# Kernel optimization log

Measured on AMD Instinct MI355X. Metric: run time of the kernel, lower is better.

Reference implementation:

```python
import jax, jax.numpy as jnp
import numpy as np

N_SRC, N_DST, K = 50000, 10000, 32
IN_F, OUT_F, H, L = 256, 128, 8, 10


def setup_inputs() -> dict:
    key = jax.random.key(0)
    ks = jax.random.split(key, 12)
    s = 0.05
    return {
        "feat": jax.random.normal(ks[0], (N_SRC, IN_F), jnp.float32),
        "labels": jax.random.uniform(ks[1], (N_SRC, L), jnp.float32),
        "labels_ori": jax.random.uniform(ks[2], (N_SRC, L), jnp.float32),
        "label_rela": jax.random.uniform(ks[3], (L, L), jnp.float32),
        "W_neigh": jax.random.normal(ks[4], (IN_F, OUT_F), jnp.float32) * s,
        "b_neigh": jnp.zeros((OUT_F,), jnp.float32),
        "W_self": jax.random.normal(ks[5], (IN_F, OUT_F), jnp.float32) * s,
        "b_self": jnp.zeros((OUT_F,), jnp.float32),
        "W_attn": jax.random.normal(ks[6], (2 * OUT_F, OUT_F * H), jnp.float32) * s,
        "b_attn": jnp.zeros((OUT_F * H,), jnp.float32),
        "feat_attn_W": jax.random.normal(ks[7], (1, H, OUT_F), jnp.float32) * s,
        "eps": jnp.full((1,), 0.5, jnp.float32),
        "out_bias": jnp.zeros((OUT_F,), jnp.float32),
        "nbr_idx": jax.random.randint(ks[8], (N_DST, K), 0, N_SRC, jnp.int32),
    }


def reference(feat, labels, labels_ori, label_rela, W_neigh, b_neigh, W_self,
              b_self, W_attn, b_attn, feat_attn_W, eps, out_bias, nbr_idx):
    n_dst = nbr_idx.shape[0]
    # lin_before_mp is True (in_feats > out_feats): fc_neigh applied to src feats
    h_src = feat @ W_neigh + b_neigh                      # (N_SRC, OUT_F)
    feat_dst = feat[:n_dst]
    cent_l = labels[:n_dst]                                # dst predicted labels
    cent_f = h_src[:n_dst]                                 # dst 'f' field
    # mailbox gather: fixed-fanout neighbors
    h = h_src[nbr_idx]                                     # (N, K, OUT_F)
    l_pred = labels[nbr_idx]                               # (N, K, L)
    # label similarity: sum(outer(l_pred_j, cent_l_i) * R)
    label_sim = jnp.einsum('nka,ab,nb->nk', l_pred, label_rela, cent_l)
    # feature attention score
    h_act = jax.nn.leaky_relu(h, negative_slope=0.1)
    cent_rep = jnp.broadcast_to(cent_f[:, None, :], h_act.shape)
    x = jnp.concatenate([h_act, cent_rep], axis=-1)        # (N, K, 2*OUT_F)
    t = (x @ W_attn + b_attn).reshape(n_dst, K, H, OUT_F)
    feat_sim = jnp.einsum('nkhd,hd->nk', t, feat_attn_W[0])
    # merge (torch.tensor(...) in the original detaches this from the graph)
    merge = jax.lax.stop_gradient(label_sim * eps[0] + feat_sim * (1.0 - eps[0]))
    att = jax.nn.softmax(merge, axis=1)                    # (N, K)
    neigh = (h * att[:, :, None]).mean(axis=1)             # (N, OUT_F)
    rst = (feat_dst @ W_self + b_self + neigh) * 0.5 + out_bias
    return rst, cent_l, labels_ori[:n_dst]
```

## Files before the change

### kernel.cpp

```cpp
#include <hip/hip_runtime.h>
#include <hip/hip_bf16.h>

#define N_SRC 50000
#define N_DST 10000
#define KNBR  32
#define IN_F  256
#define OUT_F 128
#define LDIM  10
#define ATTN_OUT 1024
#define NB2_BIG  1563
#define NB2_SELF 313
#define NB2_TOT  1876

using f32x4 = __attribute__((ext_vector_type(4))) float;
using s16x8 = __attribute__((ext_vector_type(8))) short;

#define OUT_CENT (N_DST*OUT_F)
#define OUT_LORI (N_DST*OUT_F + N_DST*LDIM)

#define WS_WCOMB 0
#define WS_BN    128
#define WS_BS    (128 + 16384)
#define WS_HSRC  (128 + 32768)
#define WS_SELF0 (WS_HSRC + (N_SRC*OUT_F/2))
#define WS_SCORE (WS_SELF0 + N_DST*OUT_F)

__device__ __forceinline__ ushort f2bf(float x) {
  __hip_bfloat16 h = __float2bfloat16(x);
  return *reinterpret_cast<ushort*>(&h);
}

__device__ __forceinline__ void unpack8(uint4 hv, float* o) {
  o[0] = __uint_as_float(hv.x << 16);
  o[1] = __uint_as_float(hv.x & 0xffff0000u);
  o[2] = __uint_as_float(hv.y << 16);
  o[3] = __uint_as_float(hv.y & 0xffff0000u);
  o[4] = __uint_as_float(hv.z << 16);
  o[5] = __uint_as_float(hv.z & 0xffff0000u);
  o[6] = __uint_as_float(hv.w << 16);
  o[7] = __uint_as_float(hv.w & 0xffff0000u);
}

__global__ __launch_bounds__(256) void prep_kernel(
    const float* __restrict__ W_attn, const float* __restrict__ fW,
    const float* __restrict__ W_neigh, const float* __restrict__ W_self,
    float* __restrict__ w_comb, ushort* __restrict__ Bn, ushort* __restrict__ Bs) {
  const int b = blockIdx.x;
  const int t = threadIdx.x;
  if (b < 128) {
    __shared__ float red[256];
    float s = 0.f;
#pragma unroll
    for (int i = 0; i < 4; ++i) {
      int o = t + i * 256;
      s += W_attn[(size_t)b * ATTN_OUT + o] * fW[o];
    }
    red[t] = s;
    __syncthreads();
    for (int st = 128; st > 0; st >>= 1) {
      if (t < st) red[t] += red[t + st];
      __syncthreads();
    }
    if (t == 0) w_comb[b] = red[0];
  } else if (b < 256) {
    int k = 2 * (b - 128) + (t >> 7);
    int n = t & 127;
    Bn[(k >> 3) * 1024 + n * 8 + (k & 7)] = f2bf(W_neigh[(size_t)k * OUT_F + n]);
  } else {
    int k = 2 * (b - 256) + (t >> 7);
    int n = t & 127;
    Bs[(k >> 3) * 1024 + n * 8 + (k & 7)] = f2bf(W_self[(size_t)k * OUT_F + n]);
  }
}

template<bool OUT_BF16>
__device__ __forceinline__ void gemm_body(
    const float* __restrict__ A, const ushort* __restrict__ Bp,
    const float* __restrict__ bias, const float* __restrict__ w_comb,
    void* __restrict__ C, float* __restrict__ score_f, int M, int m0) {
  const int t = threadIdx.x;
  const int wv = t >> 6, ln = t & 63;
  const int dg = ln & 15, kg = ln >> 4;
  int r = m0 + wv * 16 + dg;
  r = r < M ? r : M - 1;
  const float* arow = &A[(size_t)r * IN_F];

  s16x8 afr[8];
#pragma unroll
  for (int half = 0; half < 2; ++half) {
    f32x4 araw[8];
#pragma unroll
    for (int k0 = 0; k0 < 4; ++k0) {
      const f32x4* ap = (const f32x4*)&arow[(half * 4 + k0) * 32 + kg * 8];
      araw[2 * k0]     = ap[0];
      araw[2 * k0 + 1] = ap[1];
    }
#pragma unroll
    for (int k0 = 0; k0 < 4; ++k0) {
      s16x8 f;
      f[0] = (short)f2bf(araw[2*k0][0]); f[1] = (short)f2bf(araw[2*k0][1]);
      f[2] = (short)f2bf(araw[2*k0][2]); f[3] = (short)f2bf(araw[2*k0][3]);
      f[4] = (short)f2bf(araw[2*k0+1][0]); f[5] = (short)f2bf(araw[2*k0+1][1]);
      f[6] = (short)f2bf(araw[2*k0+1][2]); f[7] = (short)f2bf(araw[2*k0+1][3]);
      afr[half * 4 + k0] = f;
    }
  }

  f32x4 acc[8];
#pragma unroll
  for (int ct = 0; ct < 8; ++ct) acc[ct] = (f32x4){0.f, 0.f, 0.f, 0.f};
#pragma unroll
  for (int k0 = 0; k0 < 8; ++k0) {
    const ushort* bb = Bp + (k0 * 4 + kg) * 1024 + dg * 8;
#pragma unroll
    for (int ct = 0; ct < 8; ++ct) {
      s16x8 bfr = *reinterpret_cast<const s16x8*>(bb + ct * 128);
      acc[ct] = __builtin_amdgcn_mfma_f32_16x16x32_bf16(afr[k0], bfr, acc[ct], 0, 0, 0);
    }
  }

  float sc[4] = {0.f, 0.f, 0.f, 0.f};
#pragma unroll
  for (int ct = 0; ct < 8; ++ct) {
    int col = ct * 16 + dg;
    float bb = bias[col];
    float wc = OUT_BF16 ? w_comb[col] : 0.f;
#pragma unroll
    for (int e = 0; e < 4; ++e) {
      int rr = m0 + wv * 16 + kg * 4 + e;
      float v = acc[ct][e] + bb;
      if (OUT_BF16) {
        sc[e] = fmaf(fmaxf(v, 0.1f * v), wc, sc[e]);
        if (rr < M) ((ushort*)C)[(size_t)rr * OUT_F + col] = f2bf(v);
      } else {
        if (rr < M) ((float*)C)[(size_t)rr * OUT_F + col] = v;
      }
    }
  }
  if (OUT_BF16) {
#pragma unroll
    for (int s = 1; s < 16; s <<= 1) {
#pragma unroll
      for (int e = 0; e < 4; ++e) sc[e] += __shfl_xor(sc[e], s);
    }
    if (dg == 0) {
#pragma unroll
      for (int e = 0; e < 4; ++e) {
        int rr = m0 + wv * 16 + kg * 4 + e;
        if (rr < M) score_f[rr] = sc[e];
      }
    }
  }
}

__global__ __launch_bounds__(128, 4) void fused_gemm(
    const float* __restrict__ A,
    const ushort* __restrict__ Bn, const ushort* __restrict__ Bs,
    const float* __restrict__ bias_n, const float* __restrict__ bias_s,
    const float* __restrict__ w_comb,
    ushort* __restrict__ hsrc, float* __restrict__ self0, float* __restrict__ score_f) {
  if (blockIdx.x < NB2_BIG)
    gemm_body<true>(A, Bn, bias_n, w_comb, (void*)hsrc, score_f, N_SRC, blockIdx.x * 32);
  else
    gemm_body<false>(A, Bs, bias_s, w_comb, (void*)self0, score_f, N_DST,
                     (blockIdx.x - NB2_BIG) * 32);
}

__global__ __launch_bounds__(256, 6) void attn_kernel(
    const float* __restrict__ labels, const float* __restrict__ labels_ori,
    const float* __restrict__ label_rela, const int* __restrict__ nbr_idx,
    const ushort* __restrict__ hsrc, const float* __restrict__ self0,
    const float* __restrict__ score_f, const float* __restrict__ eps_p,
    const float* __restrict__ out_bias, float* __restrict__ out) {
  const int t = threadIdx.x;
  const int wv = t >> 6, ln = t & 63;
  const int n = blockIdx.x * 4 + wv;
  const int dg = ln & 15, kg = ln >> 4;

  const float eps = eps_p[0];
  const float om = 1.f - eps;

  float va = 0.f;
  if (dg < LDIM) {
#pragma unroll
    for (int b = 0; b < LDIM; ++b)
      va += label_rela[dg * LDIM + b] * labels[(size_t)n * LDIM + b];
    va *= eps;
  }

  const int* irow = nbr_idx + (size_t)n * KNBR;
  int ids[8];
  uint4 hv[8];
#pragma unroll
  for (int j = 0; j < 8; ++j) {
    ids[j] = irow[kg * 8 + j];
    hv[j] = *(const uint4*)(hsrc + (size_t)ids[j] * OUT_F + dg * 8);
  }
  float m[8];
#pragma unroll
  for (int j = 0; j < 8; ++j) {
    float sp = 0.f;
    if (dg == 0) sp = om * score_f[ids[j]];
    if (dg < LDIM) sp = fmaf(labels[(size_t)ids[j] * LDIM + dg], va, sp);
    m[j] = sp;
  }
#pragma unroll
  for (int s = 1; s < 16; s <<= 1) {
#pragma unroll
    for (int j = 0; j < 8; ++j) m[j] += __shfl_xor(m[j], s);
  }
  float mx = m[0];
#pragma unroll
  for (int j = 1; j < 8; ++j) mx = fmaxf(mx, m[j]);
  mx = fmaxf(mx, __shfl_xor(mx, 16));
  mx = fmaxf(mx, __shfl_xor(mx, 32));
  float ssum = 0.f;
#pragma unroll
  for (int j = 0; j < 8; ++j) {
    m[j] = __expf(m[j] - mx);
    ssum += m[j];
  }
  ssum += __shfl_xor(ssum, 16);
  ssum += __shfl_xor(ssum, 32);
  const float scale = 1.f / (ssum * (float)KNBR);
  float pn[8];
#pragma unroll
  for (int e = 0; e < 8; ++e) pn[e] = 0.f;
#pragma unroll
  for (int j = 0; j < 8; ++j) {
    float a = m[j];
    float hfj[8];
    unpack8(hv[j], hfj);
#pragma unroll
    for (int e = 0; e < 8; ++e) pn[e] = fmaf(a, hfj[e], pn[e]);
  }
#pragma unroll
  for (int e = 0; e < 8; ++e) {
    pn[e] += __shfl_xor(pn[e], 16);
    pn[e] += __shfl_xor(pn[e], 32);
  }
  if (kg == 0) {
    const float* srow = self0 + (size_t)n * OUT_F + dg * 8;
    float* orow = out + (size_t)n * OUT_F + dg * 8;
    f32x4 o0, o1;
#pragma unroll
    for (int e = 0; e < 4; ++e)
      o0[e] = (srow[e] + pn[e] * scale) * 0.5f + out_bias[dg * 8 + e];
#pragma unroll
    for (int e = 0; e < 4; ++e)
      o1[e] = (srow[4 + e] + pn[4 + e] * scale) * 0.5f + out_bias[dg * 8 + 4 + e];
    *(f32x4*)orow = o0;
    *(f32x4*)(orow + 4) = o1;
  }
  if (kg == 1 && dg < LDIM)
    out[OUT_CENT + (size_t)n * LDIM + dg] = labels[(size_t)n * LDIM + dg];
  if (kg == 2 && dg < LDIM)
    out[OUT_LORI + (size_t)n * LDIM + dg] = labels_ori[(size_t)n * LDIM + dg];
}

extern "C" void kernel_launch(void* const* d_in, const int* in_sizes, int n_in,
                              void* d_out, int out_size, void* d_ws, size_t ws_size,
                              hipStream_t stream) {
  const float* feat       = (const float*)d_in[0];
  const float* labels     = (const float*)d_in[1];
  const float* labels_ori = (const float*)d_in[2];
  const float* label_rela = (const float*)d_in[3];
  const float* W_neigh    = (const float*)d_in[4];
  const float* b_neigh    = (const float*)d_in[5];
  const float* W_self     = (const float*)d_in[6];
  const float* b_self     = (const float*)d_in[7];
  const float* W_attn     = (const float*)d_in[8];
  const float* fW         = (const float*)d_in[10];
  const float* eps        = (const float*)d_in[11];
  const float* out_bias   = (const float*)d_in[12];
  const int*   nbr_idx    = (const int*)d_in[13];

  float* wsf = (float*)d_ws;
  float* out = (float*)d_out;

  float*  w_comb  = wsf + WS_WCOMB;
  ushort* Bn      = (ushort*)(wsf + WS_BN);
  ushort* Bsf     = (ushort*)(wsf + WS_BS);
  ushort* h_src   = (ushort*)(wsf + WS_HSRC);
  float*  self0   = wsf + WS_SELF0;
  float*  score_f = wsf + WS_SCORE;

  prep_kernel<<<384, 256, 0, stream>>>(W_attn, fW, W_neigh, W_self, w_comb, Bn, Bsf);
  fused_gemm<<<NB2_TOT, 128, 0, stream>>>(feat, Bn, Bsf, b_neigh, b_self,
                                          w_comb, h_src, self0, score_f);
  attn_kernel<<<(N_DST / 4), 256, 0, stream>>>(labels, labels_ori, label_rela, nbr_idx,
                                               h_src, self0, score_f, eps, out_bias, out);
}
```

Baseline: 58.51 us.

## Fuse weight prep into GEMM kernel with atomic counter grid barrier

```diff
diff --git a/kernel.cpp b/kernel.cpp
--- a/kernel.cpp
+++ b/kernel.cpp
@@ -11,6 +11,7 @@
 #define NB2_BIG  1563
 #define NB2_SELF 313
 #define NB2_TOT  1876
+#define NPREP    384
 
 using f32x4 = __attribute__((ext_vector_type(4))) float;
 using s16x8 = __attribute__((ext_vector_type(8))) short;
@@ -24,6 +25,7 @@
 #define WS_HSRC  (128 + 32768)
 #define WS_SELF0 (WS_HSRC + (N_SRC*OUT_F/2))
 #define WS_SCORE (WS_SELF0 + N_DST*OUT_F)
+#define WS_CNT   (WS_SCORE + N_SRC + 64)
 
 __device__ __forceinline__ ushort f2bf(float x) {
   __hip_bfloat16 h = __float2bfloat16(x);
@@ -41,46 +43,64 @@
   o[7] = __uint_as_float(hv.w & 0xffff0000u);
 }
 
-__global__ __launch_bounds__(256) void prep_kernel(
+__global__ __launch_bounds__(128, 4) void prep_gemm(
+    const float* __restrict__ A,
     const float* __restrict__ W_attn, const float* __restrict__ fW,
     const float* __restrict__ W_neigh, const float* __restrict__ W_self,
-    float* __restrict__ w_comb, ushort* __restrict__ Bn, ushort* __restrict__ Bs) {
+    const float* __restrict__ bias_n, const float* __restrict__ bias_s,
+    float* __restrict__ w_comb, ushort* __restrict__ Bn, ushort* __restrict__ Bs,
+    ushort* __restrict__ hsrc, float* __restrict__ self0, float* __restrict__ score_f,
+    uint* __restrict__ cnt) {
   const int b = blockIdx.x;
-  const int t = threadIdx.x;
-  if (b < 128) {
-    __shared__ float red[256];
-    float s = 0.f;
-#pragma unroll
-    for (int i = 0; i < 4; ++i) {
-      int o = t + i * 256;
-      s += W_attn[(size_t)b * ATTN_OUT + o] * fW[o];
-    }
-    red[t] = s;
-    __syncthreads();
-    for (int st = 128; st > 0; st >>= 1) {
-      if (t < st) red[t] += red[t + st];
-      __syncthreads();
-    }
-    if (t == 0) w_comb[b] = red[0];
-  } else if (b < 256) {
-    int k = 2 * (b - 128) + (t >> 7);
-    int n = t & 127;
-    Bn[(k >> 3) * 1024 + n * 8 + (k & 7)] = f2bf(W_neigh[(size_t)k * OUT_F + n]);
-  } else {
-    int k = 2 * (b - 256) + (t >> 7);
-    int n = t & 127;
-    Bs[(k >> 3) * 1024 + n * 8 + (k & 7)] = f2bf(W_self[(size_t)k * OUT_F + n]);
-  }
-}
-
-template<bool OUT_BF16>
-__device__ __forceinline__ void gemm_body(
-    const float* __restrict__ A, const ushort* __restrict__ Bp,
-    const float* __restrict__ bias, const float* __restrict__ w_comb,
-    void* __restrict__ C, float* __restrict__ score_f, int M, int m0) {
   const int t = threadIdx.x;
   const int wv = t >> 6, ln = t & 63;
   const int dg = ln & 15, kg = ln >> 4;
+
+  const bool neigh = b < NB2_BIG;
+  const int M = neigh ? N_SRC : N_DST;
+  const int m0 = (neigh ? b : b - NB2_BIG) * 32;
+
+  if (b < NPREP) {
+    if (b < 128) {
+      __shared__ float red[128];
+      float s = 0.f;
+#pragma unroll
+      for (int i = 0; i < 8; ++i) {
+        int o = t + i * 128;
+        s += W_attn[(size_t)b * ATTN_OUT + o] * fW[o];
+      }
+      red[t] = s;
+      __syncthreads();
+      for (int st = 64; st > 0; st >>= 1) {
+        if (t < st) red[t] += red[t + st];
+        __syncthreads();
+      }
+      if (t == 0) w_comb[b] = red[0];
+    } else if (b < 256) {
+      int k = 2 * (b - 128) + (t >> 6);
+      int n0 = (t & 63) * 2;
+      ushort* dst = (b < 256) ? Bn : Bs;
+#pragma unroll
+      for (int i = 0; i < 2; ++i) {
+        int n = n0 + i;
+        Bn[(k >> 3) * 1024 + n * 8 + (k & 7)] = f2bf(W_neigh[(size_t)k * OUT_F + n]);
+      }
+    } else {
+      int k = 2 * (b - 256) + (t >> 6);
+      int n0 = (t & 63) * 2;
+#pragma unroll
+      for (int i = 0; i < 2; ++i) {
+        int n = n0 + i;
+        Bs[(k >> 3) * 1024 + n * 8 + (k & 7)] = f2bf(W_self[(size_t)k * OUT_F + n]);
+      }
+    }
+    __syncthreads();
+    if (t == 0) {
+      __threadfence();
+      __hip_atomic_fetch_add(cnt, 1u, __ATOMIC_RELEASE, __HIP_MEMORY_SCOPE_AGENT);
+    }
+  }
+
   int r = m0 + wv * 16 + dg;
   r = r < M ? r : M - 1;
   const float* arow = &A[(size_t)r * IN_F];
@@ -106,6 +126,18 @@
     }
   }
 
+  __syncthreads();
+  if (t == 0) {
+    while (__hip_atomic_load(cnt, __ATOMIC_ACQUIRE, __HIP_MEMORY_SCOPE_AGENT) < (uint)NPREP) {
+      __builtin_amdgcn_s_sleep(2);
+    }
+    __threadfence();
+  }
+  __syncthreads();
+
+  const ushort* Bp = neigh ? Bn : Bs;
+  const float* bias = neigh ? bias_n : bias_s;
+
   f32x4 acc[8];
 #pragma unroll
   for (int ct = 0; ct < 8; ++ct) acc[ct] = (f32x4){0.f, 0.f, 0.f, 0.f};
@@ -124,20 +156,20 @@
   for (int ct = 0; ct < 8; ++ct) {
     int col = ct * 16 + dg;
     float bb = bias[col];
-    float wc = OUT_BF16 ? w_comb[col] : 0.f;
+    float wc = neigh ? w_comb[col] : 0.f;
 #pragma unroll
     for (int e = 0; e < 4; ++e) {
       int rr = m0 + wv * 16 + kg * 4 + e;
       float v = acc[ct][e] + bb;
-      if (OUT_BF16) {
+      if (neigh) {
         sc[e] = fmaf(fmaxf(v, 0.1f * v), wc, sc[e]);
-        if (rr < M) ((ushort*)C)[(size_t)rr * OUT_F + col] = f2bf(v);
+        if (rr < M) hsrc[(size_t)rr * OUT_F + col] = f2bf(v);
       } else {
-        if (rr < M) ((float*)C)[(size_t)rr * OUT_F + col] = v;
-      }
-    }
-  }
-  if (OUT_BF16) {
+        if (rr < M) self0[(size_t)rr * OUT_F + col] = v;
+      }
+    }
+  }
+  if (neigh) {
 #pragma unroll
     for (int s = 1; s < 16; s <<= 1) {
 #pragma unroll
@@ -151,19 +183,6 @@
       }
     }
   }
-}
-
-__global__ __launch_bounds__(128, 4) void fused_gemm(
-    const float* __restrict__ A,
-    const ushort* __restrict__ Bn, const ushort* __restrict__ Bs,
-    const float* __restrict__ bias_n, const float* __restrict__ bias_s,
-    const float* __restrict__ w_comb,
-    ushort* __restrict__ hsrc, float* __restrict__ self0, float* __restrict__ score_f) {
-  if (blockIdx.x < NB2_BIG)
-    gemm_body<true>(A, Bn, bias_n, w_comb, (void*)hsrc, score_f, N_SRC, blockIdx.x * 32);
-  else
-    gemm_body<false>(A, Bs, bias_s, w_comb, (void*)self0, score_f, N_DST,
-                     (blockIdx.x - NB2_BIG) * 32);
 }
 
 __global__ __launch_bounds__(256, 6) void attn_kernel(
@@ -284,10 +303,12 @@
   ushort* h_src   = (ushort*)(wsf + WS_HSRC);
   float*  self0   = wsf + WS_SELF0;
   float*  score_f = wsf + WS_SCORE;
-
-  prep_kernel<<<384, 256, 0, stream>>>(W_attn, fW, W_neigh, W_self, w_comb, Bn, Bsf);
-  fused_gemm<<<NB2_TOT, 128, 0, stream>>>(feat, Bn, Bsf, b_neigh, b_self,
-                                          w_comb, h_src, self0, score_f);
+  uint*   cnt     = (uint*)(wsf + WS_CNT);
+
+  hipMemsetAsync((void*)cnt, 0, sizeof(uint), stream);
+  prep_gemm<<<NB2_TOT, 128, 0, stream>>>(feat, W_attn, fW, W_neigh, W_self,
+                                         b_neigh, b_self, w_comb, Bn, Bsf,
+                                         h_src, self0, score_f, cnt);
   attn_kernel<<<(N_DST / 4), 256, 0, stream>>>(labels, labels_ori, label_rela, nbr_idx,
                                                h_src, self0, score_f, eps, out_bias, out);
 }
```

New measurement: 170.8 us. +191.9%, slower.
